# Kernel tuning notes

Hardware: AMD Instinct MI355X
Metric: run time of the kernel (lower is better)

The kernel has to match this reference:

```python
import jax, jax.numpy as jnp
import numpy as np
import math

B, S, E, A, H, L, V = 2, 2048, 512, 512, 8, 4, 50257
HD = A // H  # 64 per-head dim (attention_size // n_heads)
PAD = 0
EPS = 1e-5

def _sin_pe():
    pos = np.arange(S)[:, None].astype(np.float32)
    div = np.exp(np.arange(0, E, 2).astype(np.float32) * (-math.log(10000.0) / E))
    pe = np.zeros((S, E), dtype=np.float32)
    pe[:, 0::2] = np.sin(pos * div)
    pe[:, 1::2] = np.cos(pos * div)
    return jnp.asarray(pe)

PE = _sin_pe()

def setup_inputs():
    key = jax.random.key(0)
    ks = jax.random.split(key, 20)
    s = 0.02
    emb = jax.random.normal(ks[0], (V, E), jnp.float32) * s
    emb = emb.at[PAD].set(0.0)  # nn.Embedding padding_idx row is zero
    return {
        "input_ids": jax.random.randint(ks[1], (B, S), 0, V, dtype=jnp.int32),
        "attention_mask": jnp.ones((B, S), jnp.int32),
        "emb": emb,
        "Wq": jax.random.normal(ks[2], (L, H, E, HD), jnp.float32) * s,
        "Wk": jax.random.normal(ks[3], (L, H, E, HD), jnp.float32) * s,
        "Wv": jax.random.normal(ks[4], (L, H, E, HD), jnp.float32) * s,
        "Wo": jax.random.normal(ks[5], (L, A, E), jnp.float32) * s,
        "ln1_g": jnp.ones((L, E), jnp.float32),
        "ln1_b": jnp.zeros((L, E), jnp.float32),
        "ln2_g": jnp.ones((L, E), jnp.float32),
        "ln2_b": jnp.zeros((L, E), jnp.float32),
        "ff_w1": jax.random.normal(ks[6], (L, E, 4 * E), jnp.float32) * s,
        "ff_b1": jnp.zeros((L, 4 * E), jnp.float32),
        "ff_w2": jax.random.normal(ks[7], (L, 4 * E, E), jnp.float32) * s,
        "ff_b2": jnp.zeros((L, E), jnp.float32),
        "lnf_g": jnp.ones((E,), jnp.float32),
        "lnf_b": jnp.zeros((E,), jnp.float32),
        "Wout": jax.random.normal(ks[8], (E, V), jnp.float32) * s,
        "bout": jnp.zeros((V,), jnp.float32),
    }

def _ln(x, g, b):
    m = jnp.mean(x, axis=-1, keepdims=True)
    v = jnp.mean((x - m) ** 2, axis=-1, keepdims=True)
    return (x - m) / jnp.sqrt(v + EPS) * g + b

def reference(input_ids, attention_mask, emb, Wq, Wk, Wv, Wo, ln1_g, ln1_b, ln2_g, ln2_b, ff_w1, ff_b1, ff_w2, ff_b2, lnf_g, lnf_b, Wout, bout):
    # mask: padding (attention_mask==0) broadcast over queries, OR causal upper triangle
    pad = (attention_mask == 0)[:, None, :]                  # [B,1,S]
    causal = jnp.triu(jnp.ones((S, S), bool), 1)             # [S,S]
    mask = (pad | causal)[:, None, :, :]                     # [B,1,S,S]
    x = emb[input_ids] + PE[None, :S]                        # [B,S,E]
    scale = 1.0 / math.sqrt(HD)

    def block(x, p):
        wq, wk, wv, wo, g1, b1, g2, b2, w1, c1, w2, c2 = p
        xn = _ln(x, g1, b1)
        q = jnp.einsum('bse,hed->bhsd', xn, wq)
        k = jnp.einsum('bse,hed->bhsd', xn, wk)
        v = jnp.einsum('bse,hed->bhsd', xn, wv)
        scores = jnp.einsum('bhsd,bhtd->bhst', q, k) * scale  # masked_fill(-inf) then /sqrt(dk) == mask after scale
        scores = jnp.where(mask, -jnp.inf, scores)
        p_attn = jax.nn.softmax(scores, axis=-1)
        attn = jnp.einsum('bhst,bhtd->bhsd', p_attn, v)
        attn = attn.transpose(0, 2, 1, 3).reshape(B, S, A)    # concat heads
        x = x + attn @ wo                                     # residual + out proj (no bias)
        xn2 = _ln(x, g2, b2)
        h = jax.nn.gelu(xn2 @ w1 + c1, approximate=False)     # nn.GELU default (erf)
        x = x + h @ w2 + c2
        return x, None

    params = (Wq, Wk, Wv, Wo, ln1_g, ln1_b, ln2_g, ln2_b, ff_w1, ff_b1, ff_w2, ff_b2)
    x, _ = jax.lax.scan(block, x, params)
    return _ln(x, lnf_g, lnf_b) @ Wout + bout                 # [B,S,V]
```

## Files before the change

kernel.cpp:

```cpp
#include <hip/hip_runtime.h>
#include <math.h>

#define BB 2
#define SS 2048
#define EE 512
#define HH 8
#define HD 64
#define LL 4
#define VV 50257
#define NTOK (BB*SS)
#define VPAD2 50432

typedef __bf16 bf16_t;
typedef bf16_t bf16x8 __attribute__((ext_vector_type(8)));
typedef float  f32x4  __attribute__((ext_vector_type(4)));

__device__ __forceinline__ void gload_lds16(const void* g, void* l) {
  __builtin_amdgcn_global_load_lds(
      (const __attribute__((address_space(1))) void*)g,
      (__attribute__((address_space(3))) void*)l, 16, 0, 0);
}

__global__ __launch_bounds__(256) void embed_kernel(const int* __restrict__ ids,
                                                    const float* __restrict__ emb,
                                                    float* __restrict__ x) {
  int idx = blockIdx.x * 256 + threadIdx.x;
  int e   = idx & (EE - 1);
  int tok = idx >> 9;
  int s   = tok & (SS - 1);
  int id  = ids[tok];
  float freq = __expf((float)(e & ~1) * -0.01798894604f);
  float ang  = (float)s * freq;
  float pe   = (e & 1) ? __cosf(ang) : __sinf(ang);
  x[idx] = emb[(size_t)id * EE + e] + pe;
}

__global__ __launch_bounds__(256) void ln_kernel(const float* __restrict__ in,
                                                 bf16_t* __restrict__ out,
                                                 const float* __restrict__ g,
                                                 const float* __restrict__ b) {
  int wv = threadIdx.x >> 6, lane = threadIdx.x & 63;
  int row = blockIdx.x * 4 + wv;
  const float4* r = reinterpret_cast<const float4*>(in + (size_t)row * EE) + lane * 2;
  float4 v0 = r[0], v1 = r[1];
  float s = v0.x + v0.y + v0.z + v0.w + v1.x + v1.y + v1.z + v1.w;
#pragma unroll
  for (int o = 32; o > 0; o >>= 1) s += __shfl_xor(s, o);
  float mean = s * (1.f / EE);
  float d0 = v0.x-mean, d1 = v0.y-mean, d2 = v0.z-mean, d3 = v0.w-mean;
  float d4 = v1.x-mean, d5 = v1.y-mean, d6 = v1.z-mean, d7 = v1.w-mean;
  float var = d0*d0+d1*d1+d2*d2+d3*d3+d4*d4+d5*d5+d6*d6+d7*d7;
#pragma unroll
  for (int o = 32; o > 0; o >>= 1) var += __shfl_xor(var, o);
  float inv = rsqrtf(var * (1.f / EE) + 1e-5f);
  const float4* gp = reinterpret_cast<const float4*>(g) + lane * 2;
  const float4* bp = reinterpret_cast<const float4*>(b) + lane * 2;
  float4 g0 = gp[0], g1 = gp[1], b0 = bp[0], b1 = bp[1];
  bf16_t tmp[8];
  tmp[0] = (bf16_t)(d0*inv*g0.x + b0.x); tmp[1] = (bf16_t)(d1*inv*g0.y + b0.y);
  tmp[2] = (bf16_t)(d2*inv*g0.z + b0.z); tmp[3] = (bf16_t)(d3*inv*g0.w + b0.w);
  tmp[4] = (bf16_t)(d4*inv*g1.x + b1.x); tmp[5] = (bf16_t)(d5*inv*g1.y + b1.y);
  tmp[6] = (bf16_t)(d6*inv*g1.z + b1.z); tmp[7] = (bf16_t)(d7*inv*g1.w + b1.w);
  *reinterpret_cast<bf16x8*>(out + (size_t)row * EE + lane * 8) = *reinterpret_cast<bf16x8*>(tmp);
}

__device__ __forceinline__ void transpose_tile(const float* __restrict__ ip,
                                               bf16_t* __restrict__ op,
                                               int k0, int n0, int ldin, int ldout,
                                               int Nvalid, float* T) {
  int t = threadIdx.x;
  int r = t >> 2, cb = (t & 3) * 16;
#pragma unroll
  for (int i = 0; i < 16; i++) {
    int n = n0 + cb + i;
    T[r * 65 + cb + i] = (n < Nvalid) ? ip[(size_t)(k0 + r) * ldin + n] : 0.f;
  }
  __syncthreads();
  bf16_t tmp[16];
#pragma unroll
  for (int i = 0; i < 16; i++) tmp[i] = (bf16_t)T[(cb + i) * 65 + r];
  bf16_t* o = op + (size_t)(n0 + r) * ldout + k0 + cb;
  *reinterpret_cast<bf16x8*>(o)     = *reinterpret_cast<bf16x8*>(&tmp[0]);
  *reinterpret_cast<bf16x8*>(o + 8) = *reinterpret_cast<bf16x8*>(&tmp[8]);
}

__global__ __launch_bounds__(256) void wconv_kernel(const float* __restrict__ in,
                                                    bf16_t* __restrict__ out,
                                                    int ldin, int ldout, int Nvalid,
                                                    long zin, long zout) {
  __shared__ float T[64 * 65];
  transpose_tile(in + (size_t)blockIdx.z * zin, out + (size_t)blockIdx.z * zout,
                 blockIdx.x * 64, blockIdx.y * 64, ldin, ldout, Nvalid, T);
}

__global__ __launch_bounds__(256) void wconv_qkv_kernel(const float* __restrict__ Wq,
                                                        const float* __restrict__ Wk,
                                                        const float* __restrict__ Wv,
                                                        bf16_t* __restrict__ out) {
  __shared__ float T[64 * 65];
  int z = blockIdx.z;
  int l = z / 24, rem = z % 24, sec = rem >> 3, h = rem & 7;
  const float* W = sec == 0 ? Wq : (sec == 1 ? Wk : Wv);
  const float* ip = W + (size_t)(l * 8 + h) * (EE * HD);
  bf16_t* op = out + (size_t)l * (1536 * 512) + (size_t)(sec * 512 + h * 64) * 512;
  transpose_tile(ip, op, blockIdx.x * 64, 0, HD, EE, HD, T);
}

template<int MODE, int TM>
__global__ __launch_bounds__(256) void gemm_bf16(
    const bf16_t* __restrict__ A, const bf16_t* __restrict__ Bt,
    int M, int N, int K,
    const float* __restrict__ bias,
    float* __restrict__ Cf, bf16_t* __restrict__ Cb,
    bf16_t* __restrict__ qo, bf16_t* __restrict__ ko, bf16_t* __restrict__ vo) {
  constexpr int MI = TM / 32;
  constexpr int LW = MI + 4;
  __shared__ __align__(16) bf16_t As[2][TM * 64];
  __shared__ __align__(16) bf16_t Bs[2][128 * 64];
  int tid = threadIdx.x, lane = tid & 63, w = tid >> 6;
  int lr = lane & 15, lg = lane >> 4;
  int m0 = blockIdx.y * TM, n0 = blockIdx.x * 128;
  f32x4 acc[MI][4];
#pragma unroll
  for (int i = 0; i < MI; i++)
#pragma unroll
    for (int j = 0; j < 4; j++) acc[i][j] = (f32x4){0.f, 0.f, 0.f, 0.f};
  int wr = w >> 1, wc = w & 1;

  const bf16_t* Abase = A  + (size_t)(m0 + lr) * K + lg * 8;
  const bf16_t* Bbase = Bt + (size_t)(n0 + lr) * K + lg * 8;

  auto stage = [&](int buf, int k0) {
#pragma unroll
    for (int i = 0; i < MI; i++) {
      int c = w * MI + i;
      gload_lds16(Abase + (size_t)(c >> 1) * 16 * K + k0 + (c & 1) * 32,
                  (char*)&As[buf][0] + c * 1024);
    }
#pragma unroll
    for (int i = 0; i < 4; i++) {
      int c = w * 4 + i;
      gload_lds16(Bbase + (size_t)(c >> 1) * 16 * K + k0 + (c & 1) * 32,
                  (char*)&Bs[buf][0] + c * 1024);
    }
  };

  int nk = K >> 6;
  stage(0, 0);
  for (int k = 0; k < nk; k++) {
    int cur = k & 1;
    if (k + 1 < nk) {
      stage(cur ^ 1, (k + 1) << 6);
      asm volatile("s_waitcnt vmcnt(%0)" :: "i"(LW) : "memory");
    } else {
      asm volatile("s_waitcnt vmcnt(0)" ::: "memory");
    }
    __builtin_amdgcn_s_barrier();
    __builtin_amdgcn_s_setprio(1);
#pragma unroll
    for (int kk = 0; kk < 2; kk++) {
      bf16x8 afr[MI], bfr[4];
#pragma unroll
      for (int mi = 0; mi < MI; mi++)
        afr[mi] = *reinterpret_cast<const bf16x8*>(
            &As[cur][(((wr * MI + mi) << 1) + kk) * 512 + lane * 8]);
#pragma unroll
      for (int ni = 0; ni < 4; ni++)
        bfr[ni] = *reinterpret_cast<const bf16x8*>(
            &Bs[cur][(((wc * 4 + ni) << 1) + kk) * 512 + lane * 8]);
#pragma unroll
      for (int mi = 0; mi < MI; mi++)
#pragma unroll
        for (int ni = 0; ni < 4; ni++)
          acc[mi][ni] = __builtin_amdgcn_mfma_f32_16x16x32_bf16(afr[mi], bfr[ni], acc[mi][ni], 0, 0, 0);
    }
    __builtin_amdgcn_s_setprio(0);
    __builtin_amdgcn_s_barrier();
  }

#pragma unroll
  for (int mi = 0; mi < MI; mi++)
#pragma unroll
    for (int ni = 0; ni < 4; ni++) {
      int colg = n0 + wc * 64 + ni * 16 + lr;
#pragma unroll
      for (int j = 0; j < 4; j++) {
        int rowg = m0 + wr * (TM / 2) + mi * 16 + lg * 4 + j;
        float v = acc[mi][ni][j];
        if (MODE == 0) {
          int sec = colg >> 9, cc = colg & 511, hh = cc >> 6, dd = cc & 63;
          int bi = rowg >> 11, s = rowg & 2047;
          if (sec == 0)      qo[(((size_t)bi * HH + hh) * SS + s) * HD + dd] = (bf16_t)(v * 0.125f);
          else if (sec == 1) ko[(((size_t)bi * HH + hh) * SS + s) * HD + dd] = (bf16_t)v;
          else               vo[(((size_t)bi * HH + hh) * HD + dd) * SS + s] = (bf16_t)v;
        } else if (MODE == 1) {
          v += bias[colg];
          v = 0.5f * v * (1.f + erff(v * 0.70710678f));
          Cb[(size_t)rowg * N + colg] = (bf16_t)v;
        } else {
          if (bias) v += bias[colg];
          Cf[(size_t)rowg * EE + colg] += v;
        }
      }
    }
}

__global__ __launch_bounds__(512) void gemm256_out(
    const bf16_t* __restrict__ A, const bf16_t* __restrict__ Bt,
    const float* __restrict__ bias, float* __restrict__ C) {
  __shared__ __align__(16) char smem[64 * 260 * 4];
  bf16_t* As = (bf16_t*)smem;
  bf16_t* Bs = (bf16_t*)(smem + 32768);
  float*  Ep = (float*)smem;
  int tid = threadIdx.x, lane = tid & 63, w = tid >> 6;
  int lr = lane & 15, lg = lane >> 4;
  int bid = blockIdx.x;
  int n0 = (bid % 197) * 256, m0 = (bid / 197) * 256;
  int wr = w >> 2, wc = w & 3;
  f32x4 acc[8][4];
#pragma unroll
  for (int i = 0; i < 8; i++)
#pragma unroll
    for (int j = 0; j < 4; j++) acc[i][j] = (f32x4){0.f, 0.f, 0.f, 0.f};

  const bf16_t* Abase = A  + (size_t)(m0 + lr) * 512 + lg * 8;
  const bf16_t* Bbase = Bt + (size_t)(n0 + lr) * 512 + lg * 8;

  for (int k0 = 0; k0 < 512; k0 += 64) {
#pragma unroll
    for (int i = 0; i < 4; i++) {
      int c = w * 4 + i;
      gload_lds16(Abase + (size_t)(c >> 1) * 16 * 512 + k0 + (c & 1) * 32,
                  (char*)As + c * 1024);
      gload_lds16(Bbase + (size_t)(c >> 1) * 16 * 512 + k0 + (c & 1) * 32,
                  (char*)Bs + c * 1024);
    }
    __syncthreads();
#pragma unroll
    for (int kk = 0; kk < 2; kk++) {
      bf16x8 afr[8], bfr[4];
#pragma unroll
      for (int mi = 0; mi < 8; mi++)
        afr[mi] = *reinterpret_cast<const bf16x8*>(
            &As[(((wr * 8 + mi) << 1) + kk) * 512 + lane * 8]);
#pragma unroll
      for (int ni = 0; ni < 4; ni++)
        bfr[ni] = *reinterpret_cast<const bf16x8*>(
            &Bs[(((wc * 4 + ni) << 1) + kk) * 512 + lane * 8]);
#pragma unroll
      for (int mi = 0; mi < 8; mi++)
#pragma unroll
        for (int ni = 0; ni < 4; ni++)
          acc[mi][ni] = __builtin_amdgcn_mfma_f32_16x16x32_bf16(afr[mi], bfr[ni], acc[mi][ni], 0, 0, 0);
    }
    __syncthreads();
  }

  int colBase = n0 + (tid & 63) * 4;
  float b0 = 0.f, b1 = 0.f, b2 = 0.f, b3 = 0.f;
  if (colBase + 3 < VV) {
    float4 bv = *reinterpret_cast<const float4*>(bias + colBase);
    b0 = bv.x; b1 = bv.y; b2 = bv.z; b3 = bv.w;
  } else {
    if (colBase     < VV) b0 = bias[colBase];
    if (colBase + 1 < VV) b1 = bias[colBase + 1];
    if (colBase + 2 < VV) b2 = bias[colBase + 2];
  }
  int rw = tid >> 6;
  for (int ch = 0; ch < 4; ch++) {
    __syncthreads();
    if (wr == (ch >> 1)) {
      int mib = (ch & 1) * 4;
#pragma unroll
      for (int mi2 = 0; mi2 < 4; mi2++)
#pragma unroll
        for (int ni = 0; ni < 4; ni++) {
          int col = wc * 64 + ni * 16 + lr;
#pragma unroll
          for (int j = 0; j < 4; j++)
            Ep[(mi2 * 16 + lg * 4 + j) * 260 + col] = acc[mib + mi2][ni][j];
        }
    }
    __syncthreads();
#pragma unroll
    for (int pass = 0; pass < 8; pass++) {
      int r = pass * 8 + rw;
      f32x4 v = *reinterpret_cast<const f32x4*>(&Ep[r * 260 + (tid & 63) * 4]);
      v[0] += b0; v[1] += b1; v[2] += b2; v[3] += b3;
      float* dst = &C[(size_t)(m0 + ch * 64 + r) * VV + colBase];
      if (colBase + 3 < VV) {
        __builtin_nontemporal_store(v, reinterpret_cast<f32x4*>(dst));
      } else {
        if (colBase     < VV) __builtin_nontemporal_store(v[0], dst);
        if (colBase + 1 < VV) __builtin_nontemporal_store(v[1], dst + 1);
        if (colBase + 2 < VV) __builtin_nontemporal_store(v[2], dst + 2);
      }
    }
  }
}

#define QBLK 64
#define KVB 64
__global__ __launch_bounds__(256) void attn_kernel(
    const bf16_t* __restrict__ qb, const bf16_t* __restrict__ kb,
    const bf16_t* __restrict__ vT, const int* __restrict__ amask,
    bf16_t* __restrict__ ab) {
  __shared__ bf16_t Qs[QBLK][72];
  __shared__ bf16_t Ps[QBLK][72];
  __shared__ __align__(16) bf16_t Ks[2][KVB * 64];
  __shared__ __align__(16) bf16_t Vs[2][KVB * 64];
  int tid = threadIdx.x, lane = tid & 63, w = tid >> 6;
  int lr = lane & 15, lg = lane >> 4;
  int bid = blockIdx.x;
  int bh = bid & 15;
  int qi = bid >> 4;
  int qq = (qi < 16) ? qi : 47 - qi;
  int q0 = qq * QBLK;
  int b = bh >> 3, h = bh & 7;
  const bf16_t* Qg = qb + (size_t)bh * SS * HD;
  const bf16_t* Kg = kb + (size_t)bh * SS * HD;
  const bf16_t* Vg = vT + (size_t)bh * HD * SS;
  const int* am = amask + b * SS;

  {
    int r = tid >> 2, c = (tid & 3) * 16;
    const uint4* s = reinterpret_cast<const uint4*>(Qg + (size_t)(q0 + r) * HD + c);
    uint4 a0 = s[0], a1 = s[1];
    *reinterpret_cast<uint4*>(&Qs[r][c])     = a0;
    *reinterpret_cast<uint4*>(&Qs[r][c + 8]) = a1;
  }

  auto stageKV = [&](int buf, int kv0) {
#pragma unroll
    for (int i = 0; i < 4; i++) {
      int c = w * 4 + i;
      if (c < 8) {
        gload_lds16(Kg + (size_t)(kv0 + (c >> 1) * 16 + lr) * HD + (c & 1) * 32 + lg * 8,
                    (char*)&Ks[buf][0] + c * 1024);
      } else {
        int cc = c - 8;
        gload_lds16(Vg + (size_t)((cc >> 1) * 16 + lr) * SS + kv0 + (cc & 1) * 32 + lg * 8,
                    (char*)&Vs[buf][0] + cc * 1024);
      }
    }
  };

  f32x4 o[4];
  f32x4 m_run, l_run;
  m_run = (f32x4){-1e30f, -1e30f, -1e30f, -1e30f};
  l_run = (f32x4){0.f, 0.f, 0.f, 0.f};
#pragma unroll
  for (int nd = 0; nd < 4; nd++) o[nd] = (f32x4){0.f, 0.f, 0.f, 0.f};

  stageKV(0, 0);
  __syncthreads();

  int ntile = qq + 1;
  for (int t = 0; t < ntile; t++) {
    int buf = t & 1;
    int kv0 = t * KVB;
    if (t + 1 < ntile) stageKV(buf ^ 1, kv0 + KVB);

    f32x4 sc[4];
#pragma unroll
    for (int ni = 0; ni < 4; ni++) sc[ni] = (f32x4){0.f, 0.f, 0.f, 0.f};
#pragma unroll
    for (int kk = 0; kk < 2; kk++) {
      bf16x8 af = *reinterpret_cast<const bf16x8*>(&Qs[w * 16 + lr][kk * 32 + lg * 8]);
      bf16x8 bf[4];
#pragma unroll
      for (int ni = 0; ni < 4; ni++)
        bf[ni] = *reinterpret_cast<const bf16x8*>(&Ks[buf][((ni << 1) + kk) * 512 + lane * 8]);
#pragma unroll
      for (int ni = 0; ni < 4; ni++)
        sc[ni] = __builtin_amdgcn_mfma_f32_16x16x32_bf16(af, bf[ni], sc[ni], 0, 0, 0);
    }

    {
      int qrb = q0 + w * 16 + lg * 4;
      float kmv[4];
#pragma unroll
      for (int ni = 0; ni < 4; ni++) kmv[ni] = am[kv0 + ni * 16 + lr] ? 0.f : -1e30f;
#pragma unroll
      for (int ni = 0; ni < 4; ni++) {
        int kg = kv0 + ni * 16 + lr;
#pragma unroll
        for (int j = 0; j < 4; j++) {
          float s = sc[ni][j] + kmv[ni];
          sc[ni][j] = (kg <= qrb + j) ? s : -1e30f;
        }
      }
      f32x4 rmax = sc[0];
#pragma unroll
      for (int ni = 1; ni < 4; ni++)
#pragma unroll
        for (int j = 0; j < 4; j++) rmax[j] = fmaxf(rmax[j], sc[ni][j]);
#pragma unroll
      for (int msk = 1; msk <= 8; msk <<= 1)
#pragma unroll
        for (int j = 0; j < 4; j++) rmax[j] = fmaxf(rmax[j], __shfl_xor(rmax[j], msk));
      f32x4 mnew, corr;
#pragma unroll
      for (int j = 0; j < 4; j++) {
        mnew[j] = fmaxf(m_run[j], rmax[j]);
        corr[j] = __expf(m_run[j] - mnew[j]);
      }
      m_run = mnew;
      f32x4 rs = (f32x4){0.f, 0.f, 0.f, 0.f};
#pragma unroll
      for (int ni = 0; ni < 4; ni++) {
#pragma unroll
        for (int j = 0; j < 4; j++) {
          float p = __expf(sc[ni][j] - mnew[j]);
          rs[j] += p;
          Ps[w * 16 + lg * 4 + j][ni * 16 + lr] = (bf16_t)p;
        }
      }
#pragma unroll
      for (int msk = 1; msk <= 8; msk <<= 1)
#pragma unroll
        for (int j = 0; j < 4; j++) rs[j] += __shfl_xor(rs[j], msk);
#pragma unroll
      for (int j = 0; j < 4; j++) l_run[j] = l_run[j] * corr[j] + rs[j];
#pragma unroll
      for (int nd = 0; nd < 4; nd++) o[nd] = o[nd] * corr;
    }

#pragma unroll
    for (int kc = 0; kc < 2; kc++) {
      bf16x8 pa = *reinterpret_cast<const bf16x8*>(&Ps[w * 16 + lr][kc * 32 + lg * 8]);
      bf16x8 vb[4];
#pragma unroll
      for (int nd = 0; nd < 4; nd++)
        vb[nd] = *reinterpret_cast<const bf16x8*>(&Vs[buf][((nd << 1) + kc) * 512 + lane * 8]);
#pragma unroll
      for (int nd = 0; nd < 4; nd++)
        o[nd] = __builtin_amdgcn_mfma_f32_16x16x32_bf16(pa, vb[nd], o[nd], 0, 0, 0);
    }
    asm volatile("s_waitcnt vmcnt(0)" ::: "memory");
    asm volatile("s_barrier" ::: "memory");
  }

  f32x4 linv;
#pragma unroll
  for (int j = 0; j < 4; j++) linv[j] = 1.f / l_run[j];
#pragma unroll
  for (int nd = 0; nd < 4; nd++)
#pragma unroll
    for (int j = 0; j < 4; j++) {
      int rowg = b * SS + q0 + w * 16 + lg * 4 + j;
      int col = h * HD + nd * 16 + lr;
      ab[(size_t)rowg * EE + col] = (bf16_t)(o[nd][j] * linv[j]);
    }
}

extern "C" void kernel_launch(void* const* d_in, const int* in_sizes, int n_in,
                              void* d_out, int out_size, void* d_ws, size_t ws_size,
                              hipStream_t stream) {
  const int*   ids   = (const int*)d_in[0];
  const int*   amask = (const int*)d_in[1];
  const float* emb   = (const float*)d_in[2];
  const float* Wq    = (const float*)d_in[3];
  const float* Wk    = (const float*)d_in[4];
  const float* Wv    = (const float*)d_in[5];
  const float* Wo    = (const float*)d_in[6];
  const float* ln1g  = (const float*)d_in[7];
  const float* ln1b  = (const float*)d_in[8];
  const float* ln2g  = (const float*)d_in[9];
  const float* ln2b  = (const float*)d_in[10];
  const float* fw1   = (const float*)d_in[11];
  const float* fb1   = (const float*)d_in[12];
  const float* fw2   = (const float*)d_in[13];
  const float* fb2   = (const float*)d_in[14];
  const float* lnfg  = (const float*)d_in[15];
  const float* lnfb  = (const float*)d_in[16];
  const float* Wout  = (const float*)d_in[17];
  const float* bout  = (const float*)d_in[18];
  float* out = (float*)d_out;

  float*  x     = (float*)d_ws;
  bf16_t* xn    = (bf16_t*)((char*)d_ws + (8u << 20));
  bf16_t* WoutT = (bf16_t*)((char*)d_ws + (12u << 20));
  char* sc = (char*)d_out;
  bf16_t* qbuf = (bf16_t*)(sc);
  bf16_t* kbuf = (bf16_t*)(sc + 4194304);
  bf16_t* vTb  = (bf16_t*)(sc + 8388608);
  bf16_t* ab   = (bf16_t*)(sc + 12582912);
  bf16_t* hb   = (bf16_t*)(sc + 16777216);
  bf16_t* Wqkv = (bf16_t*)(sc + 33554432);
  bf16_t* WoT  = (bf16_t*)(sc + 39845888);
  bf16_t* W1T  = (bf16_t*)(sc + 41943040);
  bf16_t* W2T  = (bf16_t*)(sc + 50331648);

  wconv_qkv_kernel<<<dim3(8, 1, 96), 256, 0, stream>>>(Wq, Wk, Wv, Wqkv);
  wconv_kernel<<<dim3(8, 8, LL), 256, 0, stream>>>(Wo, WoT, 512, 512, 512,
                                                   512L * 512, 512L * 512);
  wconv_kernel<<<dim3(8, 32, LL), 256, 0, stream>>>(fw1, W1T, 2048, 512, 2048,
                                                    512L * 2048, 2048L * 512);
  wconv_kernel<<<dim3(32, 8, LL), 256, 0, stream>>>(fw2, W2T, 512, 2048, 512,
                                                    2048L * 512, 512L * 2048);
  wconv_kernel<<<dim3(8, VPAD2 / 64, 1), 256, 0, stream>>>(Wout, WoutT, VV, 512, VV, 0, 0);

  embed_kernel<<<NTOK * EE / 256, 256, 0, stream>>>(ids, emb, x);

  for (int l = 0; l < LL; l++) {
    ln_kernel<<<NTOK / 4, 256, 0, stream>>>(x, xn, ln1g + l * EE, ln1b + l * EE);
    gemm_bf16<0, 128><<<dim3(12, 32), 256, 0, stream>>>(xn, Wqkv + (size_t)l * 1536 * 512,
        NTOK, 1536, 512, nullptr, nullptr, nullptr, qbuf, kbuf, vTb);
    attn_kernel<<<dim3(512), 256, 0, stream>>>(qbuf, kbuf, vTb, amask, ab);
    gemm_bf16<2, 32><<<dim3(4, 128), 256, 0, stream>>>(ab, WoT + (size_t)l * 512 * 512,
        NTOK, 512, 512, nullptr, x, nullptr, nullptr, nullptr, nullptr);
    ln_kernel<<<NTOK / 4, 256, 0, stream>>>(x, xn, ln2g + l * EE, ln2b + l * EE);
    gemm_bf16<1, 128><<<dim3(16, 32), 256, 0, stream>>>(xn, W1T + (size_t)l * 2048 * 512,
        NTOK, 2048, 512, fb1 + l * 2048, nullptr, hb, nullptr, nullptr, nullptr);
    gemm_bf16<2, 32><<<dim3(4, 128), 256, 0, stream>>>(hb, W2T + (size_t)l * 512 * 2048,
        NTOK, 512, 2048, fb2 + l * EE, x, nullptr, nullptr, nullptr, nullptr);
  }
  ln_kernel<<<NTOK / 4, 256, 0, stream>>>(x, xn, lnfg, lnfb);
  gemm256_out<<<dim3(16 * (VPAD2 / 256)), 512, 0, stream>>>(xn, WoutT, bout, out);
}
```

Baseline: 1.281 ms.

## Fuse embedding with first layernorm, merge weight conversions, shrink GEMM row tiles

Merges the embedding and PE computation with the first layer's LN1 into one kernel, so the first ln_kernel launch and one read of x are dropped. The five weight-transpose launches are folded into a single kernel that branches on block index. The QKV and FF1 GEMMs move from 128-row to 64-row tiles, doubling grid size to fill more CUs at the cost of less reuse per block. Together these mainly cut launch count and improve occupancy for two GEMMs.

```diff
diff --git a/kernel.cpp b/kernel.cpp
--- a/kernel.cpp
+++ b/kernel.cpp
@@ -21,18 +21,45 @@
       (__attribute__((address_space(3))) void*)l, 16, 0, 0);
 }
 
-__global__ __launch_bounds__(256) void embed_kernel(const int* __restrict__ ids,
-                                                    const float* __restrict__ emb,
-                                                    float* __restrict__ x) {
-  int idx = blockIdx.x * 256 + threadIdx.x;
-  int e   = idx & (EE - 1);
-  int tok = idx >> 9;
-  int s   = tok & (SS - 1);
-  int id  = ids[tok];
-  float freq = __expf((float)(e & ~1) * -0.01798894604f);
-  float ang  = (float)s * freq;
-  float pe   = (e & 1) ? __cosf(ang) : __sinf(ang);
-  x[idx] = emb[(size_t)id * EE + e] + pe;
+__global__ __launch_bounds__(256) void embed_ln_kernel(
+    const int* __restrict__ ids, const float* __restrict__ emb,
+    const float* __restrict__ g, const float* __restrict__ b,
+    float* __restrict__ x, bf16_t* __restrict__ xn) {
+  int wv = threadIdx.x >> 6, lane = threadIdx.x & 63;
+  int row = blockIdx.x * 4 + wv;
+  int s = row & (SS - 1);
+  int id = ids[row];
+  const float* er = emb + (size_t)id * EE;
+  float v[8];
+  float sum = 0.f;
+#pragma unroll
+  for (int j = 0; j < 8; j++) {
+    int e = lane * 8 + j;
+    float freq = __expf((float)(e & ~1) * -0.01798894604f);
+    float ang  = (float)s * freq;
+    float pe   = (e & 1) ? __cosf(ang) : __sinf(ang);
+    v[j] = er[e] + pe;
+    sum += v[j];
+  }
+  float4* xp = reinterpret_cast<float4*>(x + (size_t)row * EE + lane * 8);
+  xp[0] = make_float4(v[0], v[1], v[2], v[3]);
+  xp[1] = make_float4(v[4], v[5], v[6], v[7]);
+#pragma unroll
+  for (int o = 32; o > 0; o >>= 1) sum += __shfl_xor(sum, o);
+  float mean = sum * (1.f / EE);
+  float var = 0.f;
+#pragma unroll
+  for (int j = 0; j < 8; j++) { float d = v[j] - mean; var += d * d; }
+#pragma unroll
+  for (int o = 32; o > 0; o >>= 1) var += __shfl_xor(var, o);
+  float inv = rsqrtf(var * (1.f / EE) + 1e-5f);
+  bf16_t tmp[8];
+#pragma unroll
+  for (int j = 0; j < 8; j++) {
+    int e = lane * 8 + j;
+    tmp[j] = (bf16_t)((v[j] - mean) * inv * g[e] + b[e]);
+  }
+  *reinterpret_cast<bf16x8*>(xn + (size_t)row * EE + lane * 8) = *reinterpret_cast<bf16x8*>(tmp);
 }
 
 __global__ __launch_bounds__(256) void ln_kernel(const float* __restrict__ in,
@@ -84,26 +111,41 @@
   *reinterpret_cast<bf16x8*>(o + 8) = *reinterpret_cast<bf16x8*>(&tmp[8]);
 }
 
-__global__ __launch_bounds__(256) void wconv_kernel(const float* __restrict__ in,
-                                                    bf16_t* __restrict__ out,
-                                                    int ldin, int ldout, int Nvalid,
-                                                    long zin, long zout) {
+__global__ __launch_bounds__(256) void wconv_all(
+    const float* __restrict__ Wq, const float* __restrict__ Wk,
+    const float* __restrict__ Wv, const float* __restrict__ Wo,
+    const float* __restrict__ fw1, const float* __restrict__ fw2,
+    const float* __restrict__ Wout,
+    bf16_t* Wqkv, bf16_t* WoT, bf16_t* W1T, bf16_t* W2T, bf16_t* WoutT) {
   __shared__ float T[64 * 65];
-  transpose_tile(in + (size_t)blockIdx.z * zin, out + (size_t)blockIdx.z * zout,
-                 blockIdx.x * 64, blockIdx.y * 64, ldin, ldout, Nvalid, T);
-}
-
-__global__ __launch_bounds__(256) void wconv_qkv_kernel(const float* __restrict__ Wq,
-                                                        const float* __restrict__ Wk,
-                                                        const float* __restrict__ Wv,
-                                                        bf16_t* __restrict__ out) {
-  __shared__ float T[64 * 65];
-  int z = blockIdx.z;
-  int l = z / 24, rem = z % 24, sec = rem >> 3, h = rem & 7;
-  const float* W = sec == 0 ? Wq : (sec == 1 ? Wk : Wv);
-  const float* ip = W + (size_t)(l * 8 + h) * (EE * HD);
-  bf16_t* op = out + (size_t)l * (1536 * 512) + (size_t)(sec * 512 + h * 64) * 512;
-  transpose_tile(ip, op, blockIdx.x * 64, 0, HD, EE, HD, T);
+  int bid = blockIdx.x;
+  if (bid < 768) {
+    int kx = bid & 7, z = bid >> 3;
+    int l = z / 24, rem = z % 24, sec = rem >> 3, h = rem & 7;
+    const float* W = sec == 0 ? Wq : (sec == 1 ? Wk : Wv);
+    const float* ip = W + (size_t)(l * 8 + h) * (EE * HD);
+    bf16_t* op = Wqkv + (size_t)l * (1536 * 512) + (size_t)(sec * 512 + h * 64) * 512;
+    transpose_tile(ip, op, kx * 64, 0, HD, EE, HD, T);
+  } else if (bid < 1024) {
+    int r = bid - 768;
+    int kx = r & 7, ny = (r >> 3) & 7, l = r >> 6;
+    transpose_tile(Wo + (size_t)l * 512 * 512, WoT + (size_t)l * 512 * 512,
+                   kx * 64, ny * 64, 512, 512, 512, T);
+  } else if (bid < 2048) {
+    int r = bid - 1024;
+    int kx = r & 7, ny = (r >> 3) & 31, l = r >> 8;
+    transpose_tile(fw1 + (size_t)l * 512 * 2048, W1T + (size_t)l * 2048 * 512,
+                   kx * 64, ny * 64, 2048, 512, 2048, T);
+  } else if (bid < 3072) {
+    int r = bid - 2048;
+    int kx = r & 31, ny = (r >> 5) & 7, l = r >> 8;
+    transpose_tile(fw2 + (size_t)l * 2048 * 512, W2T + (size_t)l * 512 * 2048,
+                   kx * 64, ny * 64, 512, 2048, 512, T);
+  } else {
+    int r = bid - 3072;
+    int kx = r & 7, ny = r >> 3;
+    transpose_tile(Wout, WoutT, kx * 64, ny * 64, VV, 512, VV, T);
+  }
 }
 
 template<int MODE, int TM>
@@ -492,26 +534,21 @@
   bf16_t* W1T  = (bf16_t*)(sc + 41943040);
   bf16_t* W2T  = (bf16_t*)(sc + 50331648);
 
-  wconv_qkv_kernel<<<dim3(8, 1, 96), 256, 0, stream>>>(Wq, Wk, Wv, Wqkv);
-  wconv_kernel<<<dim3(8, 8, LL), 256, 0, stream>>>(Wo, WoT, 512, 512, 512,
-                                                   512L * 512, 512L * 512);
-  wconv_kernel<<<dim3(8, 32, LL), 256, 0, stream>>>(fw1, W1T, 2048, 512, 2048,
-                                                    512L * 2048, 2048L * 512);
-  wconv_kernel<<<dim3(32, 8, LL), 256, 0, stream>>>(fw2, W2T, 512, 2048, 512,
-                                                    2048L * 512, 512L * 2048);
-  wconv_kernel<<<dim3(8, VPAD2 / 64, 1), 256, 0, stream>>>(Wout, WoutT, VV, 512, VV, 0, 0);
-
-  embed_kernel<<<NTOK * EE / 256, 256, 0, stream>>>(ids, emb, x);
+  wconv_all<<<dim3(3072 + 8 * (VPAD2 / 64)), 256, 0, stream>>>(
+      Wq, Wk, Wv, Wo, fw1, fw2, Wout, Wqkv, WoT, W1T, W2T, WoutT);
+
+  embed_ln_kernel<<<NTOK / 4, 256, 0, stream>>>(ids, emb, ln1g, ln1b, x, xn);
 
   for (int l = 0; l < LL; l++) {
-    ln_kernel<<<NTOK / 4, 256, 0, stream>>>(x, xn, ln1g + l * EE, ln1b + l * EE);
-    gemm_bf16<0, 128><<<dim3(12, 32), 256, 0, stream>>>(xn, Wqkv + (size_t)l * 1536 * 512,
+    if (l > 0)
+      ln_kernel<<<NTOK / 4, 256, 0, stream>>>(x, xn, ln1g + l * EE, ln1b + l * EE);
+    gemm_bf16<0, 64><<<dim3(12, 64), 256, 0, stream>>>(xn, Wqkv + (size_t)l * 1536 * 512,
         NTOK, 1536, 512, nullptr, nullptr, nullptr, qbuf, kbuf, vTb);
     attn_kernel<<<dim3(512), 256, 0, stream>>>(qbuf, kbuf, vTb, amask, ab);
     gemm_bf16<2, 32><<<dim3(4, 128), 256, 0, stream>>>(ab, WoT + (size_t)l * 512 * 512,
         NTOK, 512, 512, nullptr, x, nullptr, nullptr, nullptr, nullptr);
     ln_kernel<<<NTOK / 4, 256, 0, stream>>>(x, xn, ln2g + l * EE, ln2b + l * EE);
-    gemm_bf16<1, 128><<<dim3(16, 32), 256, 0, stream>>>(xn, W1T + (size_t)l * 2048 * 512,
+    gemm_bf16<1, 64><<<dim3(16, 64), 256, 0, stream>>>(xn, W1T + (size_t)l * 2048 * 512,
         NTOK, 2048, 512, fb1 + l * 2048, nullptr, hb, nullptr, nullptr, nullptr);
     gemm_bf16<2, 32><<<dim3(4, 128), 256, 0, stream>>>(hb, W2T + (size_t)l * 512 * 2048,
         NTOK, 512, 2048, fb2 + l * EE, x, nullptr, nullptr, nullptr, nullptr);
```

After: 1.290 ms. About the same (+0.7%).
